# Kernel optimization log

Hardware: AMD Instinct MI355X
Metric: run time of the kernel (lower is better)

The kernel has to match this reference:

```python
import jax, jax.numpy as jnp
import numpy as np

N = 50000          # nodes
E = 800000         # edges (before self loops)
D = 128            # features (in = out)
H = 2              # heads
L = 2              # layers
NEG_SLOPE = 0.2    # GATConv leaky_relu slope


def setup_inputs() -> dict:
    key = jax.random.key(0)
    k = jax.random.split(key, 7)
    x = jax.random.normal(k[0], (N, D), dtype=jnp.float32)
    edge_index = jax.random.randint(k[1], (2, E), 0, N, dtype=jnp.int64)
    # Per-layer GATConv params (lin shared for src/dst as in PyG single-input mode)
    s = 1.0 / np.sqrt(D)
    W = jax.random.uniform(k[2], (L, D, H * D), dtype=jnp.float32, minval=-s, maxval=s)
    att_src = jax.random.uniform(k[3], (L, H, D), dtype=jnp.float32, minval=-s, maxval=s)
    att_dst = jax.random.uniform(k[4], (L, H, D), dtype=jnp.float32, minval=-s, maxval=s)
    bias = jnp.zeros((L, D), dtype=jnp.float32)
    return {"x": x, "edge_index": edge_index, "W": W,
            "att_src": att_src, "att_dst": att_dst, "bias": bias}


def _gat_layer(x, src, dst, W, a_src, a_dst, b):
    n = x.shape[0]
    h = (x @ W).reshape(n, H, D)                    # [N,H,C]
    alpha_s = jnp.sum(h * a_src[None], axis=-1)     # [N,H]
    alpha_d = jnp.sum(h * a_dst[None], axis=-1)     # [N,H]
    e = jax.nn.leaky_relu(alpha_s[src] + alpha_d[dst], NEG_SLOPE)  # [E',H]
    # segment softmax over incoming edges of each dst node
    m = jax.ops.segment_max(e, dst, num_segments=n)
    e = jnp.exp(e - m[dst])
    z = jax.ops.segment_sum(e, dst, num_segments=n)
    alpha = e / (z[dst] + 1e-16)                    # [E',H]
    msg = h[src] * alpha[:, :, None]                # [E',H,C]
    out = jax.ops.segment_sum(msg, dst, num_segments=n)  # [N,H,C]
    return out.mean(axis=1) + b                     # concat=False -> head mean


def _l2_normalize(x, eps=1e-12):
    nrm = jnp.sqrt(jnp.sum(x * x, axis=1, keepdims=True))
    return x / jnp.maximum(nrm, eps)


def reference(x, edge_index, W, att_src, att_dst, bias):
    n = x.shape[0]
    loop = jnp.arange(n, dtype=edge_index.dtype)
    src = jnp.concatenate([edge_index[0], loop])    # add self loops
    dst = jnp.concatenate([edge_index[1], loop])
    h = x
    for l in range(L):
        h = _gat_layer(h, src, dst, W[l], att_src[l], att_dst[l], bias[l])
        h = _l2_normalize(h)
    return h
```

## Files before the change

kernel.cpp:

```cpp
#include <hip/hip_runtime.h>


#define CAP 48
#define SPILLCAP 65536
#define WTSTRIDE 34816

using short8  = __attribute__((ext_vector_type(8))) short;
using float4v = __attribute__((ext_vector_type(4))) float;

static __device__ __forceinline__ float bf2f(unsigned int u16) {
    union { unsigned int i; float f; } v; v.i = u16 << 16; return v.f;
}
static __device__ __forceinline__ float bflo(unsigned int p){
    union { unsigned int i; float f; } v; v.i = p << 16; return v.f;
}
static __device__ __forceinline__ float bfhi(unsigned int p){
    union { unsigned int i; float f; } v; v.i = p & 0xffff0000u; return v.f;
}
static __device__ __forceinline__ unsigned short f2bf(float f) {
    union { float f; unsigned int i; } v; v.f = f;
    unsigned int x = v.i;
    x += 0x7fffu + ((x >> 16) & 1u);
    return (unsigned short)(x >> 16);
}
static __device__ __forceinline__ float leaky(float x){ return x > 0.f ? x : 0.2f * x; }

__global__ __launch_bounds__(256) void k_probe_zero(const unsigned int* __restrict__ xw,
                                                    const int* __restrict__ ei,
                                                    int* __restrict__ flags,
                                                    int* __restrict__ cnt, int N) {
    int i = blockIdx.x * 256 + threadIdx.x;
    if (i < N) cnt[i * 16] = 0;
    if (blockIdx.x == 0) {
        __shared__ int insane, oddnz;
        int t = threadIdx.x;
        if (t == 0) { insane = 0; oddnz = 0; }
        __syncthreads();
        unsigned int w = xw[t];
        if (((w >> 7) & 0xFFu) >= 154u) atomicOr(&insane, 1);
        if (ei[2 * t + 1] != 0) atomicOr(&oddnz, 1);
        __syncthreads();
        if (t == 0) { flags[0] = insane ? 1 : 0; flags[1] = oddnz ? 0 : 1; flags[2] = 0; }
    }
}

static __device__ __forceinline__ int edge_dst(const int* ei, int E, int i, int is64) {
    return is64 ? ei[2 * E + 2 * i] : ei[E + i];
}
static __device__ __forceinline__ int edge_src(const int* ei, int E, int i, int is64) {
    return is64 ? ei[2 * i] : ei[i];
}

__global__ __launch_bounds__(256) void k_bucket(const int* __restrict__ ei, int E, int N,
                                                int* __restrict__ flags,
                                                int* __restrict__ cnt,
                                                int* __restrict__ bucket,
                                                int* __restrict__ spill,
                                                const void* __restrict__ W,
                                                const void* __restrict__ atts,
                                                const void* __restrict__ attd,
                                                unsigned short* __restrict__ WT) {
    int base = (blockIdx.x * 256 + threadIdx.x) * 4;
    int fx = flags[0];
    int is64 = flags[1];
#pragma unroll
    for (int jj = 0; jj < 4; jj++) {
        int i = base + jj;
        if (i < 65536) {
            int layer = i >> 15;
            int rem = i & 32767;
            int k = rem >> 8, n = rem & 255;
            int srci = layer * 32768 + k * 256 + n;
            unsigned short v;
            if (fx) v = f2bf(((const float*)W)[srci]);
            else    v = ((const unsigned short*)W)[srci];
            WT[layer * WTSTRIDE + n * 128 + k] = v;
        }
        if (i < 4096) {
            int l = i >> 11;
            int rem = i & 2047;
            int rowi = rem >> 7, k = rem & 127;
            unsigned short out = 0;
            if (rowi < 4) {
                int head = rowi & 1;
                const void* att = (rowi < 2) ? atts : attd;
                float sum = 0.f;
                if (fx) {
                    const float* Wf = (const float*)W + l * 32768 + k * 256 + head * 128;
                    const float* af = (const float*)att + l * 256 + head * 128;
                    for (int c = 0; c < 128; c++) sum += Wf[c] * af[c];
                } else {
                    const unsigned short* Wh = (const unsigned short*)W + l * 32768 + k * 256 + head * 128;
                    const unsigned short* ah = (const unsigned short*)att + l * 256 + head * 128;
                    for (int c = 0; c < 128; c++) sum += bf2f(Wh[c]) * bf2f(ah[c]);
                }
                out = f2bf(sum);
            }
            WT[l * WTSTRIDE + (256 + rowi) * 128 + k] = out;
        }
    }
    int srcs[4], dsts[4];
    bool act[4];
#pragma unroll
    for (int jj = 0; jj < 4; jj++) {
        int i = base + jj;
        act[jj] = (i < E + N);
        int s = 0, d = 0;
        if (act[jj]) {
            if (i < E) {
                s = edge_src(ei, E, i, is64);
                d = edge_dst(ei, E, i, is64);
                if ((unsigned)s >= (unsigned)N) s = 0;
                if ((unsigned)d >= (unsigned)N) d = 0;
            } else { s = d = i - E; }
        }
        srcs[jj] = s; dsts[jj] = d;
    }
    int pos[4];
#pragma unroll
    for (int jj = 0; jj < 4; jj++)
        if (act[jj]) pos[jj] = atomicAdd(&cnt[dsts[jj] * 16], 1);
#pragma unroll
    for (int jj = 0; jj < 4; jj++) {
        if (!act[jj]) continue;
        if (pos[jj] < CAP) {
            bucket[dsts[jj] * CAP + pos[jj]] = srcs[jj];
        } else {
            int sp = atomicAdd(&flags[2], 1);
            if (sp < SPILLCAP) { spill[2 * sp] = dsts[jj]; spill[2 * sp + 1] = srcs[jj]; }
        }
    }
}

__global__ __launch_bounds__(256) void k_gemm_alpha(const void* __restrict__ X,
                                                    const unsigned short* __restrict__ WT,
                                                    unsigned short* __restrict__ Hb,
                                                    float* __restrict__ as_, float* __restrict__ ad_,
                                                    int N, const int* __restrict__ flags) {
    __shared__ unsigned short cbuf[4][2][16][72];
    int fx = flags[0];
    int mt = blockIdx.x;
    int wave = threadIdx.x >> 6;
    int lane = threadIdx.x & 63;
    int r16 = lane & 15, quad = lane >> 4;
    int m0 = mt << 5;
    short8 a[2][4];
#pragma unroll
    for (int mi = 0; mi < 2; mi++) {
        int arow = m0 + mi * 16 + r16; if (arow >= N) arow = N - 1;
        if (fx) {
            const float* Xf = (const float*)X;
#pragma unroll
            for (int kk = 0; kk < 4; kk++) {
                const float4v* pv = (const float4v*)(Xf + (size_t)arow * 128 + kk * 32 + quad * 8);
                float4v lo = pv[0], hi = pv[1];
                short8 t;
                t[0] = (short)f2bf(lo[0]); t[1] = (short)f2bf(lo[1]);
                t[2] = (short)f2bf(lo[2]); t[3] = (short)f2bf(lo[3]);
                t[4] = (short)f2bf(hi[0]); t[5] = (short)f2bf(hi[1]);
                t[6] = (short)f2bf(hi[2]); t[7] = (short)f2bf(hi[3]);
                a[mi][kk] = t;
            }
        } else {
            const unsigned short* Xh = (const unsigned short*)X;
#pragma unroll
            for (int kk = 0; kk < 4; kk++)
                a[mi][kk] = *(const short8*)(Xh + (size_t)arow * 128 + kk * 32 + quad * 8);
        }
    }
#pragma unroll
    for (int nn = 0; nn < 4; nn++) {
        int nt = wave * 4 + nn;
        float4v acc0 = {0.f, 0.f, 0.f, 0.f};
        float4v acc1 = {0.f, 0.f, 0.f, 0.f};
#pragma unroll
        for (int kk = 0; kk < 4; kk++) {
            short8 b = *(const short8*)(WT + (nt * 16 + r16) * 128 + kk * 32 + quad * 8);
            acc0 = __builtin_amdgcn_mfma_f32_16x16x32_bf16(a[0][kk], b, acc0, 0, 0, 0);
            acc1 = __builtin_amdgcn_mfma_f32_16x16x32_bf16(a[1][kk], b, acc1, 0, 0, 0);
        }
#pragma unroll
        for (int r = 0; r < 4; r++) {
            cbuf[wave][0][quad * 4 + r][nn * 16 + r16] = f2bf(acc0[r]);
            cbuf[wave][1][quad * 4 + r][nn * 16 + r16] = f2bf(acc1[r]);
        }
    }
    if (wave == 0) {
        float4v acc0 = {0.f, 0.f, 0.f, 0.f};
        float4v acc1 = {0.f, 0.f, 0.f, 0.f};
#pragma unroll
        for (int kk = 0; kk < 4; kk++) {
            short8 b = *(const short8*)(WT + (256 + r16) * 128 + kk * 32 + quad * 8);
            acc0 = __builtin_amdgcn_mfma_f32_16x16x32_bf16(a[0][kk], b, acc0, 0, 0, 0);
            acc1 = __builtin_amdgcn_mfma_f32_16x16x32_bf16(a[1][kk], b, acc1, 0, 0, 0);
        }
        if (r16 < 4) {
#pragma unroll
            for (int mi = 0; mi < 2; mi++) {
                float4v acc = mi ? acc1 : acc0;
#pragma unroll
                for (int r = 0; r < 4; r++) {
                    int row = m0 + mi * 16 + quad * 4 + r;
                    if (row < N) {
                        float val = acc[r];
                        if      (r16 == 0) as_[2 * row]     = val;
                        else if (r16 == 1) as_[2 * row + 1] = val;
                        else if (r16 == 2) ad_[2 * row]     = val;
                        else               ad_[2 * row + 1] = val;
                    }
                }
            }
        }
    }
#pragma unroll
    for (int mi = 0; mi < 2; mi++) {
#pragma unroll
        for (int it = 0; it < 2; it++) {
            int idx = it * 64 + lane;
            int row = idx >> 3, chunk = idx & 7;
            uint4 v = *(const uint4*)&cbuf[wave][mi][row][chunk * 8];
            int grow = m0 + mi * 16 + row;
            if (grow < N)
                *(uint4*)(Hb + (size_t)grow * 256 + wave * 64 + chunk * 8) = v;
        }
    }
}

static __device__ __forceinline__ void acc8(float* A, float w, uint4 q) {
    A[0] += w * bflo(q.x); A[1] += w * bfhi(q.x);
    A[2] += w * bflo(q.y); A[3] += w * bfhi(q.y);
    A[4] += w * bflo(q.z); A[5] += w * bfhi(q.z);
    A[6] += w * bflo(q.w); A[7] += w * bfhi(q.w);
}

__global__ __launch_bounds__(256) void k_aggregate(const unsigned short* __restrict__ Hb,
                                                   const float* __restrict__ as_, const float* __restrict__ ad_,
                                                   const int* __restrict__ cnt, const int* __restrict__ bucket,
                                                   const void* __restrict__ bias, int layer,
                                                   const int* __restrict__ flags,
                                                   void* __restrict__ outp, int N) {
    int fx = flags[0];
    int n = blockIdx.x * 4 + (threadIdx.x >> 6);
    if (n >= N) return;
    int deg = cnt[n * 16];
    if (deg > CAP) return;
    int lane = threadIdx.x & 63;
    int g = lane >> 4;
    int gl = lane & 15;
    const int* eb = bucket + n * CAP;
    float2 adv = *(const float2*)(ad_ + 2 * n);
    float ad0 = adv.x, ad1 = adv.y;

    bool act = lane < deg;
    int s = 0; float l0 = -1e30f, l1 = -1e30f;
    if (act) {
        s = eb[lane]; if ((unsigned)s >= (unsigned)N) s = 0;
        float2 av = *(const float2*)(as_ + 2 * s);
        l0 = leaky(av.x + ad0); l1 = leaky(av.y + ad1);
    }
    float m0 = 0.f, m1 = 0.f;
    if (__any(fmaxf(l0, l1) > 30.f)) {
        m0 = l0; m1 = l1;
#pragma unroll
        for (int m = 1; m < 64; m <<= 1) { m0 = fmaxf(m0, __shfl_xor(m0, m)); m1 = fmaxf(m1, __shfl_xor(m1, m)); }
    }
    float w0 = act ? __expf(l0 - m0) : 0.f;
    float w1 = act ? __expf(l1 - m1) : 0.f;

    float acc0[8] = {0,0,0,0,0,0,0,0}, acc1[8] = {0,0,0,0,0,0,0,0};
    int e = g;
    bool v = e < deg;
    float wq0 = __shfl(w0, e), wq1 = __shfl(w1, e);
    int sq = __shfl(s, e);
    uint4 q0, q1;
    if (v) {
        const unsigned short* row = Hb + ((size_t)sq << 8);
        q0 = *(const uint4*)(row + gl * 8);
        q1 = *(const uint4*)(row + 128 + gl * 8);
    }
    while (v) {
        int en = e + 4;
        bool vn = en < deg;
        float wn0 = __shfl(w0, en & 63), wn1 = __shfl(w1, en & 63);
        int sn = __shfl(s, en & 63);
        uint4 p0, p1;
        if (vn) {
            const unsigned short* row = Hb + ((size_t)sn << 8);
            p0 = *(const uint4*)(row + gl * 8);
            p1 = *(const uint4*)(row + 128 + gl * 8);
        }
        acc8(acc0, wq0, q0);
        acc8(acc1, wq1, q1);
        e = en; v = vn; wq0 = wn0; wq1 = wn1; q0 = p0; q1 = p1;
    }

    float z0 = w0, z1 = w1;
#pragma unroll
    for (int m = 1; m < 64; m <<= 1) { z0 += __shfl_xor(z0, m); z1 += __shfl_xor(z1, m); }
    float inv0 = 1.f / (z0 + 1e-16f), inv1 = 1.f / (z1 + 1e-16f);
#pragma unroll
    for (int k = 0; k < 8; k++) {
        acc0[k] += __shfl_xor(acc0[k], 16); acc0[k] += __shfl_xor(acc0[k], 32);
        acc1[k] += __shfl_xor(acc1[k], 16); acc1[k] += __shfl_xor(acc1[k], 32);
    }

    float vv[8];
    if (fx) {
        const float* bf = (const float*)bias + layer * 128 + gl * 8;
#pragma unroll
        for (int k = 0; k < 8; k++) vv[k] = 0.5f * (acc0[k] * inv0 + acc1[k] * inv1) + bf[k];
    } else {
        const unsigned short* bh = (const unsigned short*)bias + layer * 128 + gl * 8;
        uint4 bv = *(const uint4*)bh;
        float bfv[8] = { bflo(bv.x), bfhi(bv.x), bflo(bv.y), bfhi(bv.y),
                         bflo(bv.z), bfhi(bv.z), bflo(bv.w), bfhi(bv.w) };
#pragma unroll
        for (int k = 0; k < 8; k++) vv[k] = 0.5f * (acc0[k] * inv0 + acc1[k] * inv1) + bfv[k];
    }

    float ss = 0.f;
#pragma unroll
    for (int k = 0; k < 8; k++) ss += vv[k] * vv[k];
#pragma unroll
    for (int m = 1; m < 16; m <<= 1) ss += __shfl_xor(ss, m);
    float inv = 1.f / fmaxf(sqrtf(ss), 1e-12f);

    if (lane < 16) {
        if (fx) {
            float* op = (float*)outp + (size_t)n * 128 + gl * 8;
            float4 o0 = { vv[0] * inv, vv[1] * inv, vv[2] * inv, vv[3] * inv };
            float4 o1 = { vv[4] * inv, vv[5] * inv, vv[6] * inv, vv[7] * inv };
            *(float4*)op = o0;
            *(float4*)(op + 4) = o1;
        } else {
            unsigned short* op = (unsigned short*)outp + (size_t)n * 128 + gl * 8;
            uint4 pk;
            pk.x = (unsigned int)f2bf(vv[0] * inv) | ((unsigned int)f2bf(vv[1] * inv) << 16);
            pk.y = (unsigned int)f2bf(vv[2] * inv) | ((unsigned int)f2bf(vv[3] * inv) << 16);
            pk.z = (unsigned int)f2bf(vv[4] * inv) | ((unsigned int)f2bf(vv[5] * inv) << 16);
            pk.w = (unsigned int)f2bf(vv[6] * inv) | ((unsigned int)f2bf(vv[7] * inv) << 16);
            *(uint4*)op = pk;
        }
    }
}

__global__ __launch_bounds__(256) void k_spillfix(const unsigned short* __restrict__ Hb,
                                                  const float* __restrict__ as_, const float* __restrict__ ad_,
                                                  const int* __restrict__ cnt, const int* __restrict__ bucket,
                                                  const int* __restrict__ spill, const int* __restrict__ flags,
                                                  const void* __restrict__ bias, int layer,
                                                  void* __restrict__ outp, int N) {
    if (flags[2] == 0) return;
    int fx = flags[0];
    int n = blockIdx.x * 4 + (threadIdx.x >> 6);
    if (n >= N) return;
    int deg = cnt[n * 16];
    if (deg <= CAP) return;
    int lane = threadIdx.x & 63;
    int g = lane >> 4;
    int gl = lane & 15;
    const int* eb = bucket + n * CAP;
    int sc = flags[2]; if (sc > SPILLCAP) sc = SPILLCAP;
    float2 adv = *(const float2*)(ad_ + 2 * n);
    float ad0 = adv.x, ad1 = adv.y;

    float m0 = -1e30f, m1 = -1e30f;
    for (int i = lane; i < CAP; i += 64) {
        int s = eb[i]; if ((unsigned)s >= (unsigned)N) s = 0;
        float2 av = *(const float2*)(as_ + 2 * s);
        m0 = fmaxf(m0, leaky(av.x + ad0));
        m1 = fmaxf(m1, leaky(av.y + ad1));
    }
    for (int i = lane; i < sc; i += 64) {
        if (spill[2 * i] == n) {
            int s = spill[2 * i + 1]; if ((unsigned)s >= (unsigned)N) s = 0;
            float2 av = *(const float2*)(as_ + 2 * s);
            m0 = fmaxf(m0, leaky(av.x + ad0));
            m1 = fmaxf(m1, leaky(av.y + ad1));
        }
    }
#pragma unroll
    for (int m = 1; m < 64; m <<= 1) { m0 = fmaxf(m0, __shfl_xor(m0, m)); m1 = fmaxf(m1, __shfl_xor(m1, m)); }

    float acc0[8] = {0,0,0,0,0,0,0,0}, acc1[8] = {0,0,0,0,0,0,0,0};
    float z0 = 0.f, z1 = 0.f;
    {
        bool act = lane < CAP;
        int s = 0; float w0 = 0.f, w1 = 0.f;
        if (act) {
            s = eb[lane]; if ((unsigned)s >= (unsigned)N) s = 0;
            float2 av = *(const float2*)(as_ + 2 * s);
            w0 = __expf(leaky(av.x + ad0) - m0);
            w1 = __expf(leaky(av.y + ad1) - m1);
            z0 += w0; z1 += w1;
        }
        for (int j = 0; 4 * j < CAP; j++) {
            int e = 4 * j + g;
            int sq    = __shfl(s, e);
            float wq0 = __shfl(w0, e);
            float wq1 = __shfl(w1, e);
            if (e < CAP) {
                const unsigned short* row = Hb + ((size_t)sq << 8);
                uint4 q0 = *(const uint4*)(row + gl * 8);
                uint4 q1 = *(const uint4*)(row + 128 + gl * 8);
                acc8(acc0, wq0, q0);
                acc8(acc1, wq1, q1);
            }
        }
    }
    for (int i = 0; i < sc; i++) {
        int d = spill[2 * i];
        if (d != n) continue;
        int s = spill[2 * i + 1]; if ((unsigned)s >= (unsigned)N) s = 0;
        float2 av = *(const float2*)(as_ + 2 * s);
        float w0 = __expf(leaky(av.x + ad0) - m0);
        float w1 = __expf(leaky(av.y + ad1) - m1);
        if (lane == 0) { z0 += w0; z1 += w1; }
        if (g == 0) {
            const unsigned short* row = Hb + ((size_t)s << 8);
            uint4 q0 = *(const uint4*)(row + gl * 8);
            uint4 q1 = *(const uint4*)(row + 128 + gl * 8);
            acc8(acc0, w0, q0);
            acc8(acc1, w1, q1);
        }
    }
#pragma unroll
    for (int m = 1; m < 64; m <<= 1) { z0 += __shfl_xor(z0, m); z1 += __shfl_xor(z1, m); }

    float inv0 = 1.f / (z0 + 1e-16f), inv1 = 1.f / (z1 + 1e-16f);
#pragma unroll
    for (int k = 0; k < 8; k++) {
        acc0[k] += __shfl_xor(acc0[k], 16); acc0[k] += __shfl_xor(acc0[k], 32);
        acc1[k] += __shfl_xor(acc1[k], 16); acc1[k] += __shfl_xor(acc1[k], 32);
    }
    float vv[8];
    if (fx) {
        const float* bf = (const float*)bias + layer * 128 + gl * 8;
#pragma unroll
        for (int k = 0; k < 8; k++) vv[k] = 0.5f * (acc0[k] * inv0 + acc1[k] * inv1) + bf[k];
    } else {
        const unsigned short* bh = (const unsigned short*)bias + layer * 128 + gl * 8;
        uint4 bv = *(const uint4*)bh;
        float bfv[8] = { bflo(bv.x), bfhi(bv.x), bflo(bv.y), bfhi(bv.y),
                         bflo(bv.z), bfhi(bv.z), bflo(bv.w), bfhi(bv.w) };
#pragma unroll
        for (int k = 0; k < 8; k++) vv[k] = 0.5f * (acc0[k] * inv0 + acc1[k] * inv1) + bfv[k];
    }
    float ss = 0.f;
#pragma unroll
    for (int k = 0; k < 8; k++) ss += vv[k] * vv[k];
#pragma unroll
    for (int m = 1; m < 16; m <<= 1) ss += __shfl_xor(ss, m);
    float inv = 1.f / fmaxf(sqrtf(ss), 1e-12f);
    if (lane < 16) {
        if (fx) {
            float* op = (float*)outp + (size_t)n * 128 + gl * 8;
            float4 o0 = { vv[0] * inv, vv[1] * inv, vv[2] * inv, vv[3] * inv };
            float4 o1 = { vv[4] * inv, vv[5] * inv, vv[6] * inv, vv[7] * inv };
            *(float4*)op = o0;
            *(float4*)(op + 4) = o1;
        } else {
            unsigned short* op = (unsigned short*)outp + (size_t)n * 128 + gl * 8;
            uint4 pk;
            pk.x = (unsigned int)f2bf(vv[0] * inv) | ((unsigned int)f2bf(vv[1] * inv) << 16);
            pk.y = (unsigned int)f2bf(vv[2] * inv) | ((unsigned int)f2bf(vv[3] * inv) << 16);
            pk.z = (unsigned int)f2bf(vv[4] * inv) | ((unsigned int)f2bf(vv[5] * inv) << 16);
            pk.w = (unsigned int)f2bf(vv[6] * inv) | ((unsigned int)f2bf(vv[7] * inv) << 16);
            *(uint4*)op = pk;
        }
    }
}

extern "C" void kernel_launch(void* const* d_in, const int* in_sizes, int n_in,
                              void* d_out, int out_size, void* d_ws, size_t ws_size,
                              hipStream_t stream) {
    const void* x    = d_in[0];
    const int*  ei   = (const int*)d_in[1];
    const void* W    = d_in[2];
    const void* atts = d_in[3];
    const void* attd = d_in[4];
    const void* bias = d_in[5];

    int N = in_sizes[0] / 128;
    int E = in_sizes[1] / 2;

    char* p = (char*)d_ws;
    auto alloc = [&](size_t bytes) -> char* {
        char* q = p; p += (bytes + 255) & ~(size_t)255; return q;
    };
    int* flags   = (int*)alloc(256);
    int* cnt     = (int*)alloc((size_t)N * 64);
    float* as_   = (float*)alloc((size_t)N * 2 * 4);
    float* ad_   = (float*)alloc((size_t)N * 2 * 4);
    unsigned short* wt = (unsigned short*)alloc(2 * (size_t)WTSTRIDE * 2);
    int* spill   = (int*)alloc((size_t)SPILLCAP * 2 * 4);
    int* bucket  = (int*)alloc((size_t)N * CAP * 4);
    unsigned short* hbuf = (unsigned short*)alloc((size_t)N * 256 * 2);

    k_probe_zero<<<(N + 255) / 256, 256, 0, stream>>>((const unsigned int*)x, ei, flags, cnt, N);
    int work = E + N; if (work < 65536) work = 65536;
    k_bucket<<<(work + 1023) / 1024, 256, 0, stream>>>(ei, E, N, flags, cnt, bucket, spill,
                                                       W, atts, attd, wt);

    int mtiles = (N + 31) / 32;
    int ngrp = (N + 3) / 4;
    for (int l = 0; l < 2; l++) {
        const void* xin = (l == 0) ? x : (const void*)d_out;
        k_gemm_alpha<<<mtiles, 256, 0, stream>>>(xin, wt + (size_t)l * WTSTRIDE,
                                                 hbuf, as_, ad_, N, flags);
        k_aggregate<<<ngrp, 256, 0, stream>>>(hbuf, as_, ad_, cnt, bucket,
                                              bias, l, flags, d_out, N);
        k_spillfix<<<ngrp, 256, 0, stream>>>(hbuf, as_, ad_, cnt, bucket, spill, flags,
                                             bias, l, d_out, N);
    }
}
```

Before: 325.7 us.

## Fold spill handling into aggregate kernel and store bucket indices as 16-bit

Removes the separate k_spillfix launch per layer and merges its high-degree-node path into k_aggregate as a branch on deg > CAP. This cuts a full-grid launch and its flag/count reads per layer. The per-destination source bucket is also narrowed from int to unsigned short, halving bucket write and read traffic. The narrowing only holds while node ids fit in 16 bits (N ≤ 65536), which the fixed N of 50000 satisfies.

Result: no change. 329.8 us (+1.3%).

```diff
diff --git a/kernel.cpp b/kernel.cpp
--- a/kernel.cpp
+++ b/kernel.cpp
@@ -54,7 +54,7 @@
 __global__ __launch_bounds__(256) void k_bucket(const int* __restrict__ ei, int E, int N,
                                                 int* __restrict__ flags,
                                                 int* __restrict__ cnt,
-                                                int* __restrict__ bucket,
+                                                unsigned short* __restrict__ bucket,
                                                 int* __restrict__ spill,
                                                 const void* __restrict__ W,
                                                 const void* __restrict__ atts,
@@ -124,7 +124,7 @@
     for (int jj = 0; jj < 4; jj++) {
         if (!act[jj]) continue;
         if (pos[jj] < CAP) {
-            bucket[dsts[jj] * CAP + pos[jj]] = srcs[jj];
+            bucket[dsts[jj] * CAP + pos[jj]] = (unsigned short)srcs[jj];
         } else {
             int sp = atomicAdd(&flags[2], 1);
             if (sp < SPILLCAP) { spill[2 * sp] = dsts[jj]; spill[2 * sp + 1] = srcs[jj]; }
@@ -235,7 +235,9 @@
 
 __global__ __launch_bounds__(256) void k_aggregate(const unsigned short* __restrict__ Hb,
                                                    const float* __restrict__ as_, const float* __restrict__ ad_,
-                                                   const int* __restrict__ cnt, const int* __restrict__ bucket,
+                                                   const int* __restrict__ cnt,
+                                                   const unsigned short* __restrict__ bucket,
+                                                   const int* __restrict__ spill,
                                                    const void* __restrict__ bias, int layer,
                                                    const int* __restrict__ flags,
                                                    void* __restrict__ outp, int N) {
@@ -243,60 +245,127 @@
     int n = blockIdx.x * 4 + (threadIdx.x >> 6);
     if (n >= N) return;
     int deg = cnt[n * 16];
-    if (deg > CAP) return;
     int lane = threadIdx.x & 63;
     int g = lane >> 4;
     int gl = lane & 15;
-    const int* eb = bucket + n * CAP;
+    const unsigned short* eb = bucket + (size_t)n * CAP;
     float2 adv = *(const float2*)(ad_ + 2 * n);
     float ad0 = adv.x, ad1 = adv.y;
 
-    bool act = lane < deg;
-    int s = 0; float l0 = -1e30f, l1 = -1e30f;
-    if (act) {
-        s = eb[lane]; if ((unsigned)s >= (unsigned)N) s = 0;
-        float2 av = *(const float2*)(as_ + 2 * s);
-        l0 = leaky(av.x + ad0); l1 = leaky(av.y + ad1);
-    }
-    float m0 = 0.f, m1 = 0.f;
-    if (__any(fmaxf(l0, l1) > 30.f)) {
-        m0 = l0; m1 = l1;
+    float acc0[8] = {0,0,0,0,0,0,0,0}, acc1[8] = {0,0,0,0,0,0,0,0};
+    float z0, z1;
+
+    if (deg <= CAP) {
+        bool act = lane < deg;
+        int s = 0; float l0 = -1e30f, l1 = -1e30f;
+        if (act) {
+            s = (int)eb[lane]; if ((unsigned)s >= (unsigned)N) s = 0;
+            float2 av = *(const float2*)(as_ + 2 * s);
+            l0 = leaky(av.x + ad0); l1 = leaky(av.y + ad1);
+        }
+        float m0 = 0.f, m1 = 0.f;
+        if (__any(fmaxf(l0, l1) > 30.f)) {
+            m0 = l0; m1 = l1;
+#pragma unroll
+            for (int m = 1; m < 64; m <<= 1) { m0 = fmaxf(m0, __shfl_xor(m0, m)); m1 = fmaxf(m1, __shfl_xor(m1, m)); }
+        }
+        float w0 = act ? __expf(l0 - m0) : 0.f;
+        float w1 = act ? __expf(l1 - m1) : 0.f;
+
+        int e = g;
+        bool v = e < deg;
+        float wq0 = __shfl(w0, e), wq1 = __shfl(w1, e);
+        int sq = __shfl(s, e);
+        uint4 q0, q1;
+        if (v) {
+            const unsigned short* row = Hb + ((size_t)sq << 8);
+            q0 = *(const uint4*)(row + gl * 8);
+            q1 = *(const uint4*)(row + 128 + gl * 8);
+        }
+        while (v) {
+            int en = e + 4;
+            bool vn = en < deg;
+            float wn0 = __shfl(w0, en & 63), wn1 = __shfl(w1, en & 63);
+            int sn = __shfl(s, en & 63);
+            uint4 p0, p1;
+            if (vn) {
+                const unsigned short* row = Hb + ((size_t)sn << 8);
+                p0 = *(const uint4*)(row + gl * 8);
+                p1 = *(const uint4*)(row + 128 + gl * 8);
+            }
+            acc8(acc0, wq0, q0);
+            acc8(acc1, wq1, q1);
+            e = en; v = vn; wq0 = wn0; wq1 = wn1; q0 = p0; q1 = p1;
+        }
+
+        z0 = w0; z1 = w1;
+#pragma unroll
+        for (int m = 1; m < 64; m <<= 1) { z0 += __shfl_xor(z0, m); z1 += __shfl_xor(z1, m); }
+    } else {
+        int sc = flags[2]; if (sc > SPILLCAP) sc = SPILLCAP;
+        float m0 = -1e30f, m1 = -1e30f;
+        for (int i = lane; i < CAP; i += 64) {
+            int s = (int)eb[i]; if ((unsigned)s >= (unsigned)N) s = 0;
+            float2 av = *(const float2*)(as_ + 2 * s);
+            m0 = fmaxf(m0, leaky(av.x + ad0));
+            m1 = fmaxf(m1, leaky(av.y + ad1));
+        }
+        for (int i = lane; i < sc; i += 64) {
+            if (spill[2 * i] == n) {
+                int s = spill[2 * i + 1]; if ((unsigned)s >= (unsigned)N) s = 0;
+                float2 av = *(const float2*)(as_ + 2 * s);
+                m0 = fmaxf(m0, leaky(av.x + ad0));
+                m1 = fmaxf(m1, leaky(av.y + ad1));
+            }
+        }
 #pragma unroll
         for (int m = 1; m < 64; m <<= 1) { m0 = fmaxf(m0, __shfl_xor(m0, m)); m1 = fmaxf(m1, __shfl_xor(m1, m)); }
-    }
-    float w0 = act ? __expf(l0 - m0) : 0.f;
-    float w1 = act ? __expf(l1 - m1) : 0.f;
-
-    float acc0[8] = {0,0,0,0,0,0,0,0}, acc1[8] = {0,0,0,0,0,0,0,0};
-    int e = g;
-    bool v = e < deg;
-    float wq0 = __shfl(w0, e), wq1 = __shfl(w1, e);
-    int sq = __shfl(s, e);
-    uint4 q0, q1;
-    if (v) {
-        const unsigned short* row = Hb + ((size_t)sq << 8);
-        q0 = *(const uint4*)(row + gl * 8);
-        q1 = *(const uint4*)(row + 128 + gl * 8);
-    }
-    while (v) {
-        int en = e + 4;
-        bool vn = en < deg;
-        float wn0 = __shfl(w0, en & 63), wn1 = __shfl(w1, en & 63);
-        int sn = __shfl(s, en & 63);
-        uint4 p0, p1;
-        if (vn) {
-            const unsigned short* row = Hb + ((size_t)sn << 8);
-            p0 = *(const uint4*)(row + gl * 8);
-            p1 = *(const uint4*)(row + 128 + gl * 8);
-        }
-        acc8(acc0, wq0, q0);
-        acc8(acc1, wq1, q1);
-        e = en; v = vn; wq0 = wn0; wq1 = wn1; q0 = p0; q1 = p1;
-    }
-
-    float z0 = w0, z1 = w1;
-#pragma unroll
-    for (int m = 1; m < 64; m <<= 1) { z0 += __shfl_xor(z0, m); z1 += __shfl_xor(z1, m); }
+
+        z0 = 0.f; z1 = 0.f;
+        {
+            bool act = lane < CAP;
+            int s = 0; float w0 = 0.f, w1 = 0.f;
+            if (act) {
+                s = (int)eb[lane]; if ((unsigned)s >= (unsigned)N) s = 0;
+                float2 av = *(const float2*)(as_ + 2 * s);
+                w0 = __expf(leaky(av.x + ad0) - m0);
+                w1 = __expf(leaky(av.y + ad1) - m1);
+                z0 += w0; z1 += w1;
+            }
+            for (int j = 0; 4 * j < CAP; j++) {
+                int e = 4 * j + g;
+                int sq    = __shfl(s, e);
+                float wq0 = __shfl(w0, e);
+                float wq1 = __shfl(w1, e);
+                if (e < CAP) {
+                    const unsigned short* row = Hb + ((size_t)sq << 8);
+                    uint4 q0 = *(const uint4*)(row + gl * 8);
+                    uint4 q1 = *(const uint4*)(row + 128 + gl * 8);
+                    acc8(acc0, wq0, q0);
+                    acc8(acc1, wq1, q1);
+                }
+            }
+        }
+        for (int i = 0; i < sc; i++) {
+            int d = spill[2 * i];
+            if (d != n) continue;
+            int s = spill[2 * i + 1]; if ((unsigned)s >= (unsigned)N) s = 0;
+            float2 av = *(const float2*)(as_ + 2 * s);
+            float w0 = __expf(leaky(av.x + ad0) - m0);
+            float w1 = __expf(leaky(av.y + ad1) - m1);
+            if (lane == 0) { z0 += w0; z1 += w1; }
+            if (g == 0) {
+                const unsigned short* row = Hb + ((size_t)s << 8);
+                uint4 q0 = *(const uint4*)(row + gl * 8);
+                uint4 q1 = *(const uint4*)(row + 128 + gl * 8);
+                acc8(acc0, w0, q0);
+                acc8(acc1, w1, q1);
+            }
+        }
+#pragma unroll
+        for (int m = 1; m < 64; m <<= 1) { z0 += __shfl_xor(z0, m); z1 += __shfl_xor(z1, m); }
+    }
+
     float inv0 = 1.f / (z0 + 1e-16f), inv1 = 1.f / (z1 + 1e-16f);
 #pragma unroll
     for (int k = 0; k < 8; k++) {
@@ -344,133 +413,6 @@
     }
 }
 
-__global__ __launch_bounds__(256) void k_spillfix(const unsigned short* __restrict__ Hb,
-                                                  const float* __restrict__ as_, const float* __restrict__ ad_,
-                                                  const int* __restrict__ cnt, const int* __restrict__ bucket,
-                                                  const int* __restrict__ spill, const int* __restrict__ flags,
-                                                  const void* __restrict__ bias, int layer,
-                                                  void* __restrict__ outp, int N) {
-    if (flags[2] == 0) return;
-    int fx = flags[0];
-    int n = blockIdx.x * 4 + (threadIdx.x >> 6);
-    if (n >= N) return;
-    int deg = cnt[n * 16];
-    if (deg <= CAP) return;
-    int lane = threadIdx.x & 63;
-    int g = lane >> 4;
-    int gl = lane & 15;
-    const int* eb = bucket + n * CAP;
-    int sc = flags[2]; if (sc > SPILLCAP) sc = SPILLCAP;
-    float2 adv = *(const float2*)(ad_ + 2 * n);
-    float ad0 = adv.x, ad1 = adv.y;
-
-    float m0 = -1e30f, m1 = -1e30f;
-    for (int i = lane; i < CAP; i += 64) {
-        int s = eb[i]; if ((unsigned)s >= (unsigned)N) s = 0;
-        float2 av = *(const float2*)(as_ + 2 * s);
-        m0 = fmaxf(m0, leaky(av.x + ad0));
-        m1 = fmaxf(m1, leaky(av.y + ad1));
-    }
-    for (int i = lane; i < sc; i += 64) {
-        if (spill[2 * i] == n) {
-            int s = spill[2 * i + 1]; if ((unsigned)s >= (unsigned)N) s = 0;
-            float2 av = *(const float2*)(as_ + 2 * s);
-            m0 = fmaxf(m0, leaky(av.x + ad0));
-            m1 = fmaxf(m1, leaky(av.y + ad1));
-        }
-    }
-#pragma unroll
-    for (int m = 1; m < 64; m <<= 1) { m0 = fmaxf(m0, __shfl_xor(m0, m)); m1 = fmaxf(m1, __shfl_xor(m1, m)); }
-
-    float acc0[8] = {0,0,0,0,0,0,0,0}, acc1[8] = {0,0,0,0,0,0,0,0};
-    float z0 = 0.f, z1 = 0.f;
-    {
-        bool act = lane < CAP;
-        int s = 0; float w0 = 0.f, w1 = 0.f;
-        if (act) {
-            s = eb[lane]; if ((unsigned)s >= (unsigned)N) s = 0;
-            float2 av = *(const float2*)(as_ + 2 * s);
-            w0 = __expf(leaky(av.x + ad0) - m0);
-            w1 = __expf(leaky(av.y + ad1) - m1);
-            z0 += w0; z1 += w1;
-        }
-        for (int j = 0; 4 * j < CAP; j++) {
-            int e = 4 * j + g;
-            int sq    = __shfl(s, e);
-            float wq0 = __shfl(w0, e);
-            float wq1 = __shfl(w1, e);
-            if (e < CAP) {
-                const unsigned short* row = Hb + ((size_t)sq << 8);
-                uint4 q0 = *(const uint4*)(row + gl * 8);
-                uint4 q1 = *(const uint4*)(row + 128 + gl * 8);
-                acc8(acc0, wq0, q0);
-                acc8(acc1, wq1, q1);
-            }
-        }
-    }
-    for (int i = 0; i < sc; i++) {
-        int d = spill[2 * i];
-        if (d != n) continue;
-        int s = spill[2 * i + 1]; if ((unsigned)s >= (unsigned)N) s = 0;
-        float2 av = *(const float2*)(as_ + 2 * s);
-        float w0 = __expf(leaky(av.x + ad0) - m0);
-        float w1 = __expf(leaky(av.y + ad1) - m1);
-        if (lane == 0) { z0 += w0; z1 += w1; }
-        if (g == 0) {
-            const unsigned short* row = Hb + ((size_t)s << 8);
-            uint4 q0 = *(const uint4*)(row + gl * 8);
-            uint4 q1 = *(const uint4*)(row + 128 + gl * 8);
-            acc8(acc0, w0, q0);
-            acc8(acc1, w1, q1);
-        }
-    }
-#pragma unroll
-    for (int m = 1; m < 64; m <<= 1) { z0 += __shfl_xor(z0, m); z1 += __shfl_xor(z1, m); }
-
-    float inv0 = 1.f / (z0 + 1e-16f), inv1 = 1.f / (z1 + 1e-16f);
-#pragma unroll
-    for (int k = 0; k < 8; k++) {
-        acc0[k] += __shfl_xor(acc0[k], 16); acc0[k] += __shfl_xor(acc0[k], 32);
-        acc1[k] += __shfl_xor(acc1[k], 16); acc1[k] += __shfl_xor(acc1[k], 32);
-    }
-    float vv[8];
-    if (fx) {
-        const float* bf = (const float*)bias + layer * 128 + gl * 8;
-#pragma unroll
-        for (int k = 0; k < 8; k++) vv[k] = 0.5f * (acc0[k] * inv0 + acc1[k] * inv1) + bf[k];
-    } else {
-        const unsigned short* bh = (const unsigned short*)bias + layer * 128 + gl * 8;
-        uint4 bv = *(const uint4*)bh;
-        float bfv[8] = { bflo(bv.x), bfhi(bv.x), bflo(bv.y), bfhi(bv.y),
-                         bflo(bv.z), bfhi(bv.z), bflo(bv.w), bfhi(bv.w) };
-#pragma unroll
-        for (int k = 0; k < 8; k++) vv[k] = 0.5f * (acc0[k] * inv0 + acc1[k] * inv1) + bfv[k];
-    }
-    float ss = 0.f;
-#pragma unroll
-    for (int k = 0; k < 8; k++) ss += vv[k] * vv[k];
-#pragma unroll
-    for (int m = 1; m < 16; m <<= 1) ss += __shfl_xor(ss, m);
-    float inv = 1.f / fmaxf(sqrtf(ss), 1e-12f);
-    if (lane < 16) {
-        if (fx) {
-            float* op = (float*)outp + (size_t)n * 128 + gl * 8;
-            float4 o0 = { vv[0] * inv, vv[1] * inv, vv[2] * inv, vv[3] * inv };
-            float4 o1 = { vv[4] * inv, vv[5] * inv, vv[6] * inv, vv[7] * inv };
-            *(float4*)op = o0;
-            *(float4*)(op + 4) = o1;
-        } else {
-            unsigned short* op = (unsigned short*)outp + (size_t)n * 128 + gl * 8;
-            uint4 pk;
-            pk.x = (unsigned int)f2bf(vv[0] * inv) | ((unsigned int)f2bf(vv[1] * inv) << 16);
-            pk.y = (unsigned int)f2bf(vv[2] * inv) | ((unsigned int)f2bf(vv[3] * inv) << 16);
-            pk.z = (unsigned int)f2bf(vv[4] * inv) | ((unsigned int)f2bf(vv[5] * inv) << 16);
-            pk.w = (unsigned int)f2bf(vv[6] * inv) | ((unsigned int)f2bf(vv[7] * inv) << 16);
-            *(uint4*)op = pk;
-        }
-    }
-}
-
 extern "C" void kernel_launch(void* const* d_in, const int* in_sizes, int n_in,
                               void* d_out, int out_size, void* d_ws, size_t ws_size,
                               hipStream_t stream) {
@@ -494,7 +436,7 @@
     float* ad_   = (float*)alloc((size_t)N * 2 * 4);
     unsigned short* wt = (unsigned short*)alloc(2 * (size_t)WTSTRIDE * 2);
     int* spill   = (int*)alloc((size_t)SPILLCAP * 2 * 4);
-    int* bucket  = (int*)alloc((size_t)N * CAP * 4);
+    unsigned short* bucket = (unsigned short*)alloc((size_t)N * CAP * 2);
     unsigned short* hbuf = (unsigned short*)alloc((size_t)N * 256 * 2);
 
     k_probe_zero<<<(N + 255) / 256, 256, 0, stream>>>((const unsigned int*)x, ei, flags, cnt, N);
@@ -508,9 +450,7 @@
         const void* xin = (l == 0) ? x : (const void*)d_out;
         k_gemm_alpha<<<mtiles, 256, 0, stream>>>(xin, wt + (size_t)l * WTSTRIDE,
                                                  hbuf, as_, ad_, N, flags);
-        k_aggregate<<<ngrp, 256, 0, stream>>>(hbuf, as_, ad_, cnt, bucket,
+        k_aggregate<<<ngrp, 256, 0, stream>>>(hbuf, as_, ad_, cnt, bucket, spill,
                                               bias, l, flags, d_out, N);
-        k_spillfix<<<ngrp, 256, 0, stream>>>(hbuf, as_, ad_, cnt, bucket, spill, flags,
-                                             bias, l, d_out, N);
-    }
-}
+    }
+}
```

## Fuse edge bucketing into layer-0 GEMM launch and store bucket indices as u16

Applied to the files above, without the earlier changes.

Weight transpose and attention-vector folding move into their own small kernel. Edge bucketing is merged into the first-layer GEMM launch as extra blocks, so the atomic-heavy bucketing can overlap the GEMM instead of running serially before it. Bucket entries become 16-bit to halve the index footprint and traffic in the aggregate kernels. Node ids up to 50000 fit in 16 bits for this N, but the format would break for graphs with more than 65535 nodes.

Result: slower. 343.0 us (+5.3%).

```diff
diff --git a/kernel.cpp b/kernel.cpp
--- a/kernel.cpp
+++ b/kernel.cpp
@@ -44,6 +44,47 @@
     }
 }
 
+__global__ __launch_bounds__(256) void k_transpose(const void* __restrict__ W,
+                                                   const void* __restrict__ atts,
+                                                   const void* __restrict__ attd,
+                                                   unsigned short* __restrict__ WT,
+                                                   const int* __restrict__ flags) {
+    int i = blockIdx.x * 256 + threadIdx.x;
+    int fx = flags[0];
+    if (i < 65536) {
+        int layer = i >> 15;
+        int rem = i & 32767;
+        int k = rem >> 8, n = rem & 255;
+        int srci = layer * 32768 + k * 256 + n;
+        unsigned short v;
+        if (fx) v = f2bf(((const float*)W)[srci]);
+        else    v = ((const unsigned short*)W)[srci];
+        WT[layer * WTSTRIDE + n * 128 + k] = v;
+    }
+    if (i < 4096) {
+        int l = i >> 11;
+        int rem = i & 2047;
+        int rowi = rem >> 7, k = rem & 127;
+        unsigned short out = 0;
+        if (rowi < 4) {
+            int head = rowi & 1;
+            const void* att = (rowi < 2) ? atts : attd;
+            float sum = 0.f;
+            if (fx) {
+                const float* Wf = (const float*)W + l * 32768 + k * 256 + head * 128;
+                const float* af = (const float*)att + l * 256 + head * 128;
+                for (int c = 0; c < 128; c++) sum += Wf[c] * af[c];
+            } else {
+                const unsigned short* Wh = (const unsigned short*)W + l * 32768 + k * 256 + head * 128;
+                const unsigned short* ah = (const unsigned short*)att + l * 256 + head * 128;
+                for (int c = 0; c < 128; c++) sum += bf2f(Wh[c]) * bf2f(ah[c]);
+            }
+            out = f2bf(sum);
+        }
+        WT[l * WTSTRIDE + (256 + rowi) * 128 + k] = out;
+    }
+}
+
 static __device__ __forceinline__ int edge_dst(const int* ei, int E, int i, int is64) {
     return is64 ? ei[2 * E + 2 * i] : ei[E + i];
 }
@@ -51,95 +92,12 @@
     return is64 ? ei[2 * i] : ei[i];
 }
 
-__global__ __launch_bounds__(256) void k_bucket(const int* __restrict__ ei, int E, int N,
-                                                int* __restrict__ flags,
-                                                int* __restrict__ cnt,
-                                                int* __restrict__ bucket,
-                                                int* __restrict__ spill,
-                                                const void* __restrict__ W,
-                                                const void* __restrict__ atts,
-                                                const void* __restrict__ attd,
-                                                unsigned short* __restrict__ WT) {
-    int base = (blockIdx.x * 256 + threadIdx.x) * 4;
-    int fx = flags[0];
-    int is64 = flags[1];
-#pragma unroll
-    for (int jj = 0; jj < 4; jj++) {
-        int i = base + jj;
-        if (i < 65536) {
-            int layer = i >> 15;
-            int rem = i & 32767;
-            int k = rem >> 8, n = rem & 255;
-            int srci = layer * 32768 + k * 256 + n;
-            unsigned short v;
-            if (fx) v = f2bf(((const float*)W)[srci]);
-            else    v = ((const unsigned short*)W)[srci];
-            WT[layer * WTSTRIDE + n * 128 + k] = v;
-        }
-        if (i < 4096) {
-            int l = i >> 11;
-            int rem = i & 2047;
-            int rowi = rem >> 7, k = rem & 127;
-            unsigned short out = 0;
-            if (rowi < 4) {
-                int head = rowi & 1;
-                const void* att = (rowi < 2) ? atts : attd;
-                float sum = 0.f;
-                if (fx) {
-                    const float* Wf = (const float*)W + l * 32768 + k * 256 + head * 128;
-                    const float* af = (const float*)att + l * 256 + head * 128;
-                    for (int c = 0; c < 128; c++) sum += Wf[c] * af[c];
-                } else {
-                    const unsigned short* Wh = (const unsigned short*)W + l * 32768 + k * 256 + head * 128;
-                    const unsigned short* ah = (const unsigned short*)att + l * 256 + head * 128;
-                    for (int c = 0; c < 128; c++) sum += bf2f(Wh[c]) * bf2f(ah[c]);
-                }
-                out = f2bf(sum);
-            }
-            WT[l * WTSTRIDE + (256 + rowi) * 128 + k] = out;
-        }
-    }
-    int srcs[4], dsts[4];
-    bool act[4];
-#pragma unroll
-    for (int jj = 0; jj < 4; jj++) {
-        int i = base + jj;
-        act[jj] = (i < E + N);
-        int s = 0, d = 0;
-        if (act[jj]) {
-            if (i < E) {
-                s = edge_src(ei, E, i, is64);
-                d = edge_dst(ei, E, i, is64);
-                if ((unsigned)s >= (unsigned)N) s = 0;
-                if ((unsigned)d >= (unsigned)N) d = 0;
-            } else { s = d = i - E; }
-        }
-        srcs[jj] = s; dsts[jj] = d;
-    }
-    int pos[4];
-#pragma unroll
-    for (int jj = 0; jj < 4; jj++)
-        if (act[jj]) pos[jj] = atomicAdd(&cnt[dsts[jj] * 16], 1);
-#pragma unroll
-    for (int jj = 0; jj < 4; jj++) {
-        if (!act[jj]) continue;
-        if (pos[jj] < CAP) {
-            bucket[dsts[jj] * CAP + pos[jj]] = srcs[jj];
-        } else {
-            int sp = atomicAdd(&flags[2], 1);
-            if (sp < SPILLCAP) { spill[2 * sp] = dsts[jj]; spill[2 * sp + 1] = srcs[jj]; }
-        }
-    }
-}
-
-__global__ __launch_bounds__(256) void k_gemm_alpha(const void* __restrict__ X,
-                                                    const unsigned short* __restrict__ WT,
-                                                    unsigned short* __restrict__ Hb,
-                                                    float* __restrict__ as_, float* __restrict__ ad_,
-                                                    int N, const int* __restrict__ flags) {
-    __shared__ unsigned short cbuf[4][2][16][72];
-    int fx = flags[0];
-    int mt = blockIdx.x;
+static __device__ __forceinline__ void gemm_body(int mt, const void* __restrict__ X,
+                                                 const unsigned short* __restrict__ WT,
+                                                 unsigned short* __restrict__ Hb,
+                                                 float* __restrict__ as_, float* __restrict__ ad_,
+                                                 int N, int fx,
+                                                 unsigned short (*cbuf)[2][16][72]) {
     int wave = threadIdx.x >> 6;
     int lane = threadIdx.x & 63;
     int r16 = lane & 15, quad = lane >> 4;
@@ -226,6 +184,74 @@
     }
 }
 
+static __device__ __forceinline__ void bucket_body(int bblk, const int* __restrict__ ei,
+                                                   int E, int N,
+                                                   int* __restrict__ flags,
+                                                   int* __restrict__ cnt,
+                                                   unsigned short* __restrict__ bucket,
+                                                   int* __restrict__ spill) {
+    int base = (bblk * 256 + (int)threadIdx.x) * 4;
+    int is64 = flags[1];
+    int srcs[4], dsts[4];
+    bool act[4];
+#pragma unroll
+    for (int jj = 0; jj < 4; jj++) {
+        int i = base + jj;
+        act[jj] = (i < E + N);
+        int s = 0, d = 0;
+        if (act[jj]) {
+            if (i < E) {
+                s = edge_src(ei, E, i, is64);
+                d = edge_dst(ei, E, i, is64);
+                if ((unsigned)s >= (unsigned)N) s = 0;
+                if ((unsigned)d >= (unsigned)N) d = 0;
+            } else { s = d = i - E; }
+        }
+        srcs[jj] = s; dsts[jj] = d;
+    }
+    int pos[4];
+#pragma unroll
+    for (int jj = 0; jj < 4; jj++)
+        if (act[jj]) pos[jj] = atomicAdd(&cnt[dsts[jj] * 16], 1);
+#pragma unroll
+    for (int jj = 0; jj < 4; jj++) {
+        if (!act[jj]) continue;
+        if (pos[jj] < CAP) {
+            bucket[(size_t)dsts[jj] * CAP + pos[jj]] = (unsigned short)srcs[jj];
+        } else {
+            int sp = atomicAdd(&flags[2], 1);
+            if (sp < SPILLCAP) { spill[2 * sp] = dsts[jj]; spill[2 * sp + 1] = srcs[jj]; }
+        }
+    }
+}
+
+__global__ __launch_bounds__(256) void k_gemm_bucket(const void* __restrict__ X,
+                                                     const unsigned short* __restrict__ WT,
+                                                     unsigned short* __restrict__ Hb,
+                                                     float* __restrict__ as_, float* __restrict__ ad_,
+                                                     int N, int E, int mtiles,
+                                                     const int* __restrict__ ei,
+                                                     int* __restrict__ flags,
+                                                     int* __restrict__ cnt,
+                                                     unsigned short* __restrict__ bucket,
+                                                     int* __restrict__ spill) {
+    __shared__ unsigned short cbuf[4][2][16][72];
+    if ((int)blockIdx.x < mtiles) {
+        gemm_body(blockIdx.x, X, WT, Hb, as_, ad_, N, flags[0], cbuf);
+    } else {
+        bucket_body(blockIdx.x - mtiles, ei, E, N, flags, cnt, bucket, spill);
+    }
+}
+
+__global__ __launch_bounds__(256) void k_gemm_alpha(const void* __restrict__ X,
+                                                    const unsigned short* __restrict__ WT,
+                                                    unsigned short* __restrict__ Hb,
+                                                    float* __restrict__ as_, float* __restrict__ ad_,
+                                                    int N, const int* __restrict__ flags) {
+    __shared__ unsigned short cbuf[4][2][16][72];
+    gemm_body(blockIdx.x, X, WT, Hb, as_, ad_, N, flags[0], cbuf);
+}
+
 static __device__ __forceinline__ void acc8(float* A, float w, uint4 q) {
     A[0] += w * bflo(q.x); A[1] += w * bfhi(q.x);
     A[2] += w * bflo(q.y); A[3] += w * bfhi(q.y);
@@ -235,7 +261,8 @@
 
 __global__ __launch_bounds__(256) void k_aggregate(const unsigned short* __restrict__ Hb,
                                                    const float* __restrict__ as_, const float* __restrict__ ad_,
-                                                   const int* __restrict__ cnt, const int* __restrict__ bucket,
+                                                   const int* __restrict__ cnt,
+                                                   const unsigned short* __restrict__ bucket,
                                                    const void* __restrict__ bias, int layer,
                                                    const int* __restrict__ flags,
                                                    void* __restrict__ outp, int N) {
@@ -247,14 +274,14 @@
     int lane = threadIdx.x & 63;
     int g = lane >> 4;
     int gl = lane & 15;
-    const int* eb = bucket + n * CAP;
+    const unsigned short* eb = bucket + (size_t)n * CAP;
     float2 adv = *(const float2*)(ad_ + 2 * n);
     float ad0 = adv.x, ad1 = adv.y;
 
     bool act = lane < deg;
     int s = 0; float l0 = -1e30f, l1 = -1e30f;
     if (act) {
-        s = eb[lane]; if ((unsigned)s >= (unsigned)N) s = 0;
+        s = (int)eb[lane]; if ((unsigned)s >= (unsigned)N) s = 0;
         float2 av = *(const float2*)(as_ + 2 * s);
         l0 = leaky(av.x + ad0); l1 = leaky(av.y + ad1);
     }
@@ -346,7 +373,8 @@
 
 __global__ __launch_bounds__(256) void k_spillfix(const unsigned short* __restrict__ Hb,
                                                   const float* __restrict__ as_, const float* __restrict__ ad_,
-                                                  const int* __restrict__ cnt, const int* __restrict__ bucket,
+                                                  const int* __restrict__ cnt,
+                                                  const unsigned short* __restrict__ bucket,
                                                   const int* __restrict__ spill, const int* __restrict__ flags,
                                                   const void* __restrict__ bias, int layer,
                                                   void* __restrict__ outp, int N) {
@@ -359,14 +387,14 @@
     int lane = threadIdx.x & 63;
     int g = lane >> 4;
     int gl = lane & 15;
-    const int* eb = bucket + n * CAP;
+    const unsigned short* eb = bucket + (size_t)n * CAP;
     int sc = flags[2]; if (sc > SPILLCAP) sc = SPILLCAP;
     float2 adv = *(const float2*)(ad_ + 2 * n);
     float ad0 = adv.x, ad1 = adv.y;
 
     float m0 = -1e30f, m1 = -1e30f;
     for (int i = lane; i < CAP; i += 64) {
-        int s = eb[i]; if ((unsigned)s >= (unsigned)N) s = 0;
+        int s = (int)eb[i]; if ((unsigned)s >= (unsigned)N) s = 0;
         float2 av = *(const float2*)(as_ + 2 * s);
         m0 = fmaxf(m0, leaky(av.x + ad0));
         m1 = fmaxf(m1, leaky(av.y + ad1));
@@ -388,7 +416,7 @@
         bool act = lane < CAP;
         int s = 0; float w0 = 0.f, w1 = 0.f;
         if (act) {
-            s = eb[lane]; if ((unsigned)s >= (unsigned)N) s = 0;
+            s = (int)eb[lane]; if ((unsigned)s >= (unsigned)N) s = 0;
             float2 av = *(const float2*)(as_ + 2 * s);
             w0 = __expf(leaky(av.x + ad0) - m0);
             w1 = __expf(leaky(av.y + ad1) - m1);
@@ -494,23 +522,27 @@
     float* ad_   = (float*)alloc((size_t)N * 2 * 4);
     unsigned short* wt = (unsigned short*)alloc(2 * (size_t)WTSTRIDE * 2);
     int* spill   = (int*)alloc((size_t)SPILLCAP * 2 * 4);
-    int* bucket  = (int*)alloc((size_t)N * CAP * 4);
+    unsigned short* bucket = (unsigned short*)alloc((size_t)N * CAP * 2);
     unsigned short* hbuf = (unsigned short*)alloc((size_t)N * 256 * 2);
 
     k_probe_zero<<<(N + 255) / 256, 256, 0, stream>>>((const unsigned int*)x, ei, flags, cnt, N);
-    int work = E + N; if (work < 65536) work = 65536;
-    k_bucket<<<(work + 1023) / 1024, 256, 0, stream>>>(ei, E, N, flags, cnt, bucket, spill,
-                                                       W, atts, attd, wt);
+    k_transpose<<<256, 256, 0, stream>>>(W, atts, attd, wt, flags);
 
     int mtiles = (N + 31) / 32;
+    int bblocks = (E + N + 1023) / 1024;
     int ngrp = (N + 3) / 4;
-    for (int l = 0; l < 2; l++) {
-        const void* xin = (l == 0) ? x : (const void*)d_out;
-        k_gemm_alpha<<<mtiles, 256, 0, stream>>>(xin, wt + (size_t)l * WTSTRIDE,
-                                                 hbuf, as_, ad_, N, flags);
-        k_aggregate<<<ngrp, 256, 0, stream>>>(hbuf, as_, ad_, cnt, bucket,
-                                              bias, l, flags, d_out, N);
-        k_spillfix<<<ngrp, 256, 0, stream>>>(hbuf, as_, ad_, cnt, bucket, spill, flags,
-                                             bias, l, d_out, N);
-    }
-}
+
+    k_gemm_bucket<<<mtiles + bblocks, 256, 0, stream>>>(x, wt, hbuf, as_, ad_,
+                                                        N, E, mtiles, ei, flags, cnt, bucket, spill);
+    k_aggregate<<<ngrp, 256, 0, stream>>>(hbuf, as_, ad_, cnt, bucket,
+                                          bias, 0, flags, d_out, N);
+    k_spillfix<<<ngrp, 256, 0, stream>>>(hbuf, as_, ad_, cnt, bucket, spill, flags,
+                                         bias, 0, d_out, N);
+
+    k_gemm_alpha<<<mtiles, 256, 0, stream>>>(d_out, wt + (size_t)WTSTRIDE,
+                                             hbuf, as_, ad_, N, flags);
+    k_aggregate<<<ngrp, 256, 0, stream>>>(hbuf, as_, ad_, cnt, bucket,
+                                          bias, 1, flags, d_out, N);
+    k_spillfix<<<ngrp, 256, 0, stream>>>(hbuf, as_, ad_, cnt, bucket, spill, flags,
+                                         bias, 1, d_out, N);
+}
```
